# Optimization experiments

Measured on AMD Instinct MI355X. Metric: run time of the kernel, lower is better.

Reference implementation:

```python
import jax, jax.numpy as jnp
import numpy as np

N_NODES = 10000
N_EDGES = 80000
N_GRAPHS = 64
H, D = 4, 512          # num_heads, out_feats
EMB = 768
HFEAT = 512
NCLS = 2
SLOPE = 0.2            # DGL GATConv default negative_slope
BN_EPS = 1e-5


def setup_inputs() -> dict:
    key = jax.random.key(0)
    ks = jax.random.split(key, 24)
    f32 = jnp.float32
    rn = lambda k, s, sc=0.02: jax.random.normal(k, s, dtype=f32) * sc
    inp = {
        "node_feat": jax.random.normal(ks[0], (N_NODES, EMB), dtype=f32),
        "func_feat": jax.random.normal(ks[1], (N_NODES, EMB), dtype=f32),
        "W1": rn(ks[2], (EMB, H * D)),
        "al1": rn(ks[3], (H, D), 0.1),
        "ar1": rn(ks[4], (H, D), 0.1),
        "b1": jnp.zeros((H * D,), f32),
        "W2": rn(ks[5], (H * D, H * D)),
        "al2": rn(ks[6], (H, D), 0.1),
        "ar2": rn(ks[7], (H, D), 0.1),
        "b2": jnp.zeros((H * D,), f32),
        "Wfc": rn(ks[8], (H * D, HFEAT)),
        "bfc": jnp.zeros((HFEAT,), f32),
        "Wfco": rn(ks[9], (EMB, HFEAT)),
        "bfco": jnp.zeros((HFEAT,), f32),
        "Wh": rn(ks[10], (8, HFEAT, HFEAT)),
        "bh": jnp.zeros((8, HFEAT), f32),
        "gamma": jnp.ones((HFEAT,), f32),
        "beta": jnp.zeros((HFEAT,), f32),
        "Whfc": rn(ks[11], (HFEAT, HFEAT)),
        "bhfc": jnp.zeros((HFEAT,), f32),
        "Wf": rn(ks[12], (HFEAT, NCLS)),
        "bf": jnp.zeros((NCLS,), f32),
        "src": jax.random.randint(ks[13], (N_EDGES,), 0, N_NODES),
        "dst": jax.random.randint(ks[14], (N_EDGES,), 0, N_NODES),
        "graph_id": jnp.sort(jax.random.randint(ks[15], (N_NODES,), 0, N_GRAPHS)),
    }
    return inp


def gat_conv(h, W, al, ar, b, src, dst):
    """DGL GATConv (eval mode): fc -> per-head attention logits -> edge
    softmax over incoming edges -> scatter-sum -> +bias. Returns (N, H*D)."""
    feat = (h @ W).reshape(-1, H, D)                      # (N,H,D)
    el = jnp.einsum('nhd,hd->nh', feat, al)               # (N,H)
    er = jnp.einsum('nhd,hd->nh', feat, ar)
    e = jax.nn.leaky_relu(el[src] + er[dst], SLOPE)       # (E,H)
    emax = jax.ops.segment_max(e, dst, num_segments=N_NODES)
    ex = jnp.exp(e - emax[dst])
    den = jax.ops.segment_sum(ex, dst, num_segments=N_NODES)
    a = ex / den[dst]                                     # edge softmax (E,H)
    msg = feat[src] * a[:, :, None]                       # (E,H,D) gather+weight
    out = jax.ops.segment_sum(msg, dst, num_segments=N_NODES)
    return (out + b.reshape(1, H, D)).reshape(-1, H * D)


def reference(node_feat, func_feat, W1, al1, ar1, b1, W2, al2, ar2, b2,
              Wfc, bfc, Wfco, bfco, Wh, bh, gamma, beta, Whfc, bhfc,
              Wf, bf, src, dst, graph_id):
    h = gat_conv(node_feat, W1, al1, ar1, b1, src, dst)   # (N, 2048)
    h = gat_conv(h, W2, al2, ar2, b2, src, dst)           # (N, 2048)
    h = jax.nn.elu(h @ Wfc + bfc)                         # (N, 512)
    h_func = jax.nn.elu(func_feat @ Wfco + bfco)          # (N, 512)
    for i in range(8):
        h = jax.nn.elu(h @ Wh[i] + bh[i])
        h_func = jax.nn.elu(h_func @ Wh[i] + bh[i])       # dead for output (as in torch)
    counts = jax.ops.segment_sum(jnp.ones((N_NODES,), h.dtype), graph_id,
                                 num_segments=N_GRAPHS)
    hg = jax.ops.segment_sum(h, graph_id, num_segments=N_GRAPHS)
    hg = hg / jnp.maximum(counts, 1.0)[:, None]           # dgl.mean_nodes (G, 512)
    # BatchNorm1d eval with running_mean=0, running_var=1
    hg = hg / jnp.sqrt(1.0 + BN_EPS) * gamma + beta
    hg = jax.nn.elu(hg @ Whfc + bhfc)
    return hg @ Wf + bf                                   # (G, NCLS)
```

## Files before the change

kernel.cpp:

```cpp
#include <hip/hip_runtime.h>
#include <hip/hip_bf16.h>
#include <math.h>

#define N_NODES 10000
#define N_EDGES 80000
#define N_GRAPHS 64
#define NH 4
#define HD 512
#define HDTOT 2048
#define EMB 768
#define HFEAT 512
#define MAXDEG 512

typedef _Float16 half8 __attribute__((ext_vector_type(8)));
typedef _Float16 half4 __attribute__((ext_vector_type(4)));
typedef float f32x4 __attribute__((ext_vector_type(4)));

__device__ __forceinline__ void gload_lds16(const void* g, void* l) {
  __builtin_amdgcn_global_load_lds(
      (const __attribute__((address_space(1))) unsigned int*)g,
      (__attribute__((address_space(3))) unsigned int*)l, 16, 0, 0);
}

template <int BM>
__global__ __launch_bounds__(256) void gemm_f16_kernel(
    const _Float16* __restrict__ A, const _Float16* __restrict__ BT,
    const float* __restrict__ bias, _Float16* __restrict__ C,
    int M, int N, int K, int act) {
  constexpr int WR = (BM == 128) ? 2 : 1;
  constexpr int WC = 4 / WR;
  constexpr int MI = (BM / WR) / 16;
  constexpr int NI = (128 / WC) / 16;
  constexpr int NW = NI * 16;
  constexpr int CS = NW + 4;
  constexpr int GPR = NW / 8;

  __shared__ _Float16 smem[(BM + 128) * 64];
  _Float16* As = smem;
  _Float16* Bs = smem + BM * 64;

  const int bn = blockIdx.x * 128, bm = blockIdx.y * BM;
  const int t = threadIdx.x;
  const int lane = t & 63, wave = t >> 6;
  const int wr = wave / WC, wc = wave % WC;
  const int m0 = wr * (BM / WR), n0 = wc * NW;
  const int fr = lane & 15, fq = lane >> 4;

  f32x4 acc[MI][NI];
#pragma unroll
  for (int i = 0; i < MI; ++i)
#pragma unroll
    for (int j = 0; j < NI; ++j) acc[i][j] = (f32x4){0.f, 0.f, 0.f, 0.f};

  for (int k0 = 0; k0 < K; k0 += 64) {
    __syncthreads();
#pragma unroll
    for (int it = 0; it < BM / 32; ++it) {
      int gid = it * 256 + t;
      int r = gid >> 3;
      int q = (gid & 7) ^ (r & 7);
      int grow = bm + r;
      if (grow >= M) grow = M - 1;
      gload_lds16(A + (size_t)grow * K + k0 + q * 8,
                  &As[(it * 256 + wave * 64) * 8]);
    }
#pragma unroll
    for (int it = 0; it < 4; ++it) {
      int gid = it * 256 + t;
      int r = gid >> 3;
      int q = (gid & 7) ^ (r & 7);
      gload_lds16(BT + (size_t)(bn + r) * K + k0 + q * 8,
                  &Bs[(it * 256 + wave * 64) * 8]);
    }
    __syncthreads();

#pragma unroll
    for (int kk = 0; kk < 2; ++kk) {
      half8 af[MI], bf[NI];
#pragma unroll
      for (int mi = 0; mi < MI; ++mi) {
        int m = m0 + mi * 16 + fr;
        af[mi] = *(const half8*)&As[m * 64 + (((kk * 4 + fq) ^ (m & 7))) * 8];
      }
#pragma unroll
      for (int ni = 0; ni < NI; ++ni) {
        int n = n0 + ni * 16 + fr;
        bf[ni] = *(const half8*)&Bs[n * 64 + (((kk * 4 + fq) ^ (n & 7))) * 8];
      }
#pragma unroll
      for (int mi = 0; mi < MI; ++mi)
#pragma unroll
        for (int ni = 0; ni < NI; ++ni)
          acc[mi][ni] = __builtin_amdgcn_mfma_f32_16x16x32_f16(
              af[mi], bf[ni], acc[mi][ni], 0, 0, 0);
    }
  }
  __syncthreads();
  _Float16* cs = smem + wave * 16 * CS;
#pragma unroll
  for (int mi = 0; mi < MI; ++mi) {
#pragma unroll
    for (int ni = 0; ni < NI; ++ni) {
      float bb = bias ? bias[bn + n0 + ni * 16 + fr] : 0.f;
#pragma unroll
      for (int j = 0; j < 4; ++j) {
        float v = acc[mi][ni][j] + bb;
        if (act == 1) v = v > 0.f ? v : expm1f(v);
        cs[(fq * 4 + j) * CS + ni * 16 + fr] = (_Float16)v;
      }
    }
#pragma unroll
    for (int i = 0; i < NW / 32; ++i) {
      int piece = i * 64 + lane;
      int r = piece / GPR, g = piece % GPR;
      int grow = bm + m0 + mi * 16 + r;
      if (grow < M) {
        half8 v = *(const half8*)&cs[r * CS + g * 8];
        *(half8*)&C[(size_t)grow * N + bn + n0 + g * 8] = v;
      }
    }
  }
}

__global__ __launch_bounds__(256) void convert_wt_kernel(
    const float* __restrict__ W, _Float16* __restrict__ WT, int K, int N) {
  __shared__ float tile[32][33];
  W += (size_t)blockIdx.z * K * N;
  WT += (size_t)blockIdx.z * K * N;
  int k0 = blockIdx.x * 32, n0 = blockIdx.y * 32;
  int t = threadIdx.x;
  int r = t >> 3, c4 = (t & 7) * 4;
  float4 v = *(const float4*)(W + (size_t)(k0 + r) * N + n0 + c4);
  tile[r][c4 + 0] = v.x;
  tile[r][c4 + 1] = v.y;
  tile[r][c4 + 2] = v.z;
  tile[r][c4 + 3] = v.w;
  __syncthreads();
  float x0 = tile[c4 + 0][r], x1 = tile[c4 + 1][r];
  float x2 = tile[c4 + 2][r], x3 = tile[c4 + 3][r];
  size_t o = (size_t)(n0 + r) * K + k0 + c4;
  *(half4*)&WT[o] = (half4){(_Float16)x0, (_Float16)x1, (_Float16)x2, (_Float16)x3};
}

__global__ void convert_f32_f16_kernel(const float* __restrict__ x,
                                       _Float16* __restrict__ y, int n4) {
  int gid = blockIdx.x * blockDim.x + threadIdx.x;
  if (gid >= n4) return;
  float4 v = *(const float4*)(x + gid * 4);
  *(half4*)(y + gid * 4) =
      (half4){(_Float16)v.x, (_Float16)v.y, (_Float16)v.z, (_Float16)v.w};
}

__global__ void hist_kernel(const int* __restrict__ dst, int* __restrict__ cnt, int E) {
  int gid = blockIdx.x * blockDim.x + threadIdx.x;
  if (gid < E) atomicAdd(&cnt[dst[gid]], 1);
}

__global__ void scan_kernel(const int* __restrict__ cnt, int* __restrict__ row_ptr,
                            int* __restrict__ cursor, int n) {
  __shared__ int part[256];
  int t = threadIdx.x;
  int chunk = (n + 255) / 256;
  int s0 = t * chunk;
  int s1 = min(s0 + chunk, n);
  int sum = 0;
  for (int i = s0; i < s1; ++i) sum += cnt[i];
  part[t] = sum;
  __syncthreads();
  if (t == 0) {
    int acc = 0;
    for (int i = 0; i < 256; ++i) { int v = part[i]; part[i] = acc; acc += v; }
    row_ptr[n] = acc;
  }
  __syncthreads();
  int run = part[t];
  for (int i = s0; i < s1; ++i) {
    row_ptr[i] = run;
    cursor[i] = run;
    run += cnt[i];
  }
}

__global__ void scatter_kernel(const int* __restrict__ src, const int* __restrict__ dst,
                               int* __restrict__ cursor, int* __restrict__ csr_src,
                               int E) {
  int gid = blockIdx.x * blockDim.x + threadIdx.x;
  if (gid < E) {
    int d = dst[gid];
    int pos = atomicAdd(&cursor[d], 1);
    csr_src[pos] = src[gid];
  }
}

__global__ __launch_bounds__(256) void el_er_kernel(
    const _Float16* __restrict__ feat, const float* __restrict__ al,
    const float* __restrict__ ar, float* __restrict__ el, float* __restrict__ er) {
  int n = blockIdx.x;
  int t = threadIdx.x;
  int h = t >> 6, lane = t & 63;
  half8 f = *(const half8*)(feat + (size_t)n * HDTOT + h * HD + lane * 8);
  const float* ap = al + h * HD + lane * 8;
  const float* rp = ar + h * HD + lane * 8;
  float4 a0 = *(const float4*)ap, a1 = *(const float4*)(ap + 4);
  float4 r0 = *(const float4*)rp, r1 = *(const float4*)(rp + 4);
  float f0 = (float)f[0], f1 = (float)f[1], f2 = (float)f[2], f3 = (float)f[3];
  float f4 = (float)f[4], f5 = (float)f[5], f6 = (float)f[6], f7 = (float)f[7];
  float sl = f0 * a0.x + f1 * a0.y + f2 * a0.z + f3 * a0.w +
             f4 * a1.x + f5 * a1.y + f6 * a1.z + f7 * a1.w;
  float sr = f0 * r0.x + f1 * r0.y + f2 * r0.z + f3 * r0.w +
             f4 * r1.x + f5 * r1.y + f6 * r1.z + f7 * r1.w;
  for (int off = 32; off; off >>= 1) {
    sl += __shfl_down(sl, off);
    sr += __shfl_down(sr, off);
  }
  if (lane == 0) {
    el[n * NH + h] = sl;
    er[n * NH + h] = sr;
  }
}

__global__ __launch_bounds__(256) void softmax_aggregate_kernel(
    const _Float16* __restrict__ feat, const float* __restrict__ el,
    const float* __restrict__ er, const int* __restrict__ row_ptr,
    const int* __restrict__ csr_src, float* __restrict__ e_buf,
    const float* __restrict__ bias, _Float16* __restrict__ out) {
  __shared__ float wl[NH][MAXDEG];
  int n = blockIdx.x;
  int t = threadIdx.x;
  int h = t >> 6, lane = t & 63;
  int s = row_ptr[n], epos = row_ptr[n + 1];
  int deg = epos - s;
  bool lds_w = (deg <= MAXDEG);

  if (deg > 0) {
    float ern = er[n * NH + h];
    if (deg <= 64) {
      int p = s + lane;
      bool on = lane < deg;
      float logit = 0.f;
      float m = -INFINITY;
      if (on) {
        float v = el[csr_src[p] * NH + h] + ern;
        logit = v >= 0.f ? v : 0.2f * v;
        m = logit;
      }
#pragma unroll
      for (int off = 32; off; off >>= 1) m = fmaxf(m, __shfl_xor(m, off));
      float ex = on ? expf(logit - m) : 0.f;
      float sum = ex;
#pragma unroll
      for (int off = 32; off; off >>= 1) sum += __shfl_xor(sum, off);
      float inv = 1.f / sum;
      if (on) wl[h][lane] = ex * inv;
    } else if (lds_w) {
      float m = -INFINITY;
      for (int p = s + lane; p < epos; p += 64) {
        float v = el[csr_src[p] * NH + h] + ern;
        v = v >= 0.f ? v : 0.2f * v;
        wl[h][p - s] = v;
        m = fmaxf(m, v);
      }
      for (int off = 32; off; off >>= 1) m = fmaxf(m, __shfl_xor(m, off));
      float sum = 0.f;
      for (int p = s + lane; p < epos; p += 64) {
        float ex = expf(wl[h][p - s] - m);
        wl[h][p - s] = ex;
        sum += ex;
      }
      for (int off = 32; off; off >>= 1) sum += __shfl_xor(sum, off);
      float inv = 1.f / sum;
      for (int p = s + lane; p < epos; p += 64) wl[h][p - s] *= inv;
    } else {
      float m = -INFINITY;
      for (int p = s + lane; p < epos; p += 64) {
        float v = el[csr_src[p] * NH + h] + ern;
        v = v >= 0.f ? v : 0.2f * v;
        e_buf[p * NH + h] = v;
        m = fmaxf(m, v);
      }
      for (int off = 32; off; off >>= 1) m = fmaxf(m, __shfl_xor(m, off));
      float sum = 0.f;
      for (int p = s + lane; p < epos; p += 64) {
        float ex = expf(e_buf[p * NH + h] - m);
        e_buf[p * NH + h] = ex;
        sum += ex;
      }
      for (int off = 32; off; off >>= 1) sum += __shfl_xor(sum, off);
      float inv = 1.f / sum;
      for (int p = s + lane; p < epos; p += 64) e_buf[p * NH + h] *= inv;
    }
  }
  __syncthreads();

  int base = t * 8;
  float acc[8] = {0.f, 0.f, 0.f, 0.f, 0.f, 0.f, 0.f, 0.f};
  int p = s;
  for (; p + 4 <= epos; p += 4) {
    int q = p - s;
    int sn0 = csr_src[p + 0], sn1 = csr_src[p + 1];
    int sn2 = csr_src[p + 2], sn3 = csr_src[p + 3];
    float a0 = lds_w ? wl[h][q + 0] : e_buf[(p + 0) * NH + h];
    float a1 = lds_w ? wl[h][q + 1] : e_buf[(p + 1) * NH + h];
    float a2 = lds_w ? wl[h][q + 2] : e_buf[(p + 2) * NH + h];
    float a3 = lds_w ? wl[h][q + 3] : e_buf[(p + 3) * NH + h];
    half8 f0 = *(const half8*)(feat + (size_t)sn0 * HDTOT + base);
    half8 f1 = *(const half8*)(feat + (size_t)sn1 * HDTOT + base);
    half8 f2 = *(const half8*)(feat + (size_t)sn2 * HDTOT + base);
    half8 f3 = *(const half8*)(feat + (size_t)sn3 * HDTOT + base);
#pragma unroll
    for (int i = 0; i < 8; ++i)
      acc[i] += a0 * (float)f0[i] + a1 * (float)f1[i] +
                a2 * (float)f2[i] + a3 * (float)f3[i];
  }
  for (; p < epos; ++p) {
    int sn = csr_src[p];
    float a = lds_w ? wl[h][p - s] : e_buf[p * NH + h];
    half8 f = *(const half8*)(feat + (size_t)sn * HDTOT + base);
#pragma unroll
    for (int i = 0; i < 8; ++i) acc[i] += a * (float)f[i];
  }
  float4 b0 = *(const float4*)(bias + base);
  float4 b1 = *(const float4*)(bias + base + 4);
  half8 o;
  o[0] = (_Float16)(acc[0] + b0.x); o[1] = (_Float16)(acc[1] + b0.y);
  o[2] = (_Float16)(acc[2] + b0.z); o[3] = (_Float16)(acc[3] + b0.w);
  o[4] = (_Float16)(acc[4] + b1.x); o[5] = (_Float16)(acc[5] + b1.y);
  o[6] = (_Float16)(acc[6] + b1.z); o[7] = (_Float16)(acc[7] + b1.w);
  *(half8*)(out + (size_t)n * HDTOT + base) = o;
}

__global__ __launch_bounds__(512) void pool_final_kernel(
    const _Float16* __restrict__ hfeat, const int* __restrict__ graph_id,
    const float* __restrict__ gamma, const float* __restrict__ beta,
    const float* __restrict__ Whfc, const float* __restrict__ bhfc,
    const float* __restrict__ Wf, const float* __restrict__ bf,
    float* __restrict__ out) {
  __shared__ float sh[HFEAT];
  __shared__ float st[HFEAT];
  __shared__ float r0[8], r1[8];
  __shared__ int s_lo, s_hi;
  int g = blockIdx.x, t = threadIdx.x;
  if (t == 0) {
    int lo = 0, hi = N_NODES;
    while (lo < hi) { int m = (lo + hi) >> 1; if (graph_id[m] < g) lo = m + 1; else hi = m; }
    s_lo = lo;
    int lo2 = lo, hi2 = N_NODES;
    while (lo2 < hi2) { int m = (lo2 + hi2) >> 1; if (graph_id[m] < g + 1) lo2 = m + 1; else hi2 = m; }
    s_hi = lo2;
  }
  __syncthreads();
  int lo = s_lo, hi = s_hi;
  int col = t;
  float acc = 0.f;
  for (int n = lo; n < hi; ++n) acc += (float)hfeat[(size_t)n * HFEAT + col];
  float invc = 1.f / fmaxf((float)(hi - lo), 1.f);
  float bnscale = rsqrtf(1.f + 1e-5f);
  sh[col] = acc * invc * bnscale * gamma[col] + beta[col];
  __syncthreads();
  float a2 = bhfc[col];
  for (int k = 0; k < HFEAT; ++k) a2 += sh[k] * Whfc[k * HFEAT + col];
  st[col] = a2 > 0.f ? a2 : expm1f(a2);
  __syncthreads();
  float p0 = st[col] * Wf[col * 2 + 0];
  float p1 = st[col] * Wf[col * 2 + 1];
  for (int off = 32; off; off >>= 1) {
    p0 += __shfl_down(p0, off);
    p1 += __shfl_down(p1, off);
  }
  int w = t >> 6;
  if ((t & 63) == 0) { r0[w] = p0; r1[w] = p1; }
  __syncthreads();
  if (t == 0) {
    float q0 = bf[0], q1 = bf[1];
#pragma unroll
    for (int i = 0; i < 8; ++i) { q0 += r0[i]; q1 += r1[i]; }
    out[g * 2 + 0] = q0;
    out[g * 2 + 1] = q1;
  }
}

static void gemm_raw(const _Float16* A, const _Float16* wt, const float* bias,
                     _Float16* C, int M, int N, int K, int act,
                     bool small_m_tile, hipStream_t stream) {
  if (small_m_tile) {
    dim3 grid(N / 128, (M + 63) / 64);
    hipLaunchKernelGGL(gemm_f16_kernel<64>, grid, dim3(256), 0, stream,
                       A, wt, bias, C, M, N, K, act);
  } else {
    dim3 grid(N / 128, (M + 127) / 128);
    hipLaunchKernelGGL(gemm_f16_kernel<128>, grid, dim3(256), 0, stream,
                       A, wt, bias, C, M, N, K, act);
  }
}

static void gemm(const _Float16* A, const float* W, _Float16* wt,
                 const float* bias, _Float16* C, int M, int N, int K, int act,
                 bool small_m_tile, hipStream_t stream) {
  hipLaunchKernelGGL(convert_wt_kernel, dim3(K / 32, N / 32, 1), dim3(256),
                     0, stream, W, wt, K, N);
  gemm_raw(A, wt, bias, C, M, N, K, act, small_m_tile, stream);
}

static void gat_layer(const _Float16* h_in, int K_in, const float* W, _Float16* wt,
                      const float* al, const float* ar, const float* b,
                      const int* row_ptr, const int* csr_src,
                      _Float16* featbuf, float* el, float* er,
                      float* e_buf, _Float16* out, hipStream_t stream) {
  gemm(h_in, W, wt, nullptr, featbuf, N_NODES, HDTOT, K_in, 0, false, stream);
  hipLaunchKernelGGL(el_er_kernel, dim3(N_NODES), dim3(256), 0, stream, featbuf, al, ar, el, er);
  hipLaunchKernelGGL(softmax_aggregate_kernel, dim3(N_NODES), dim3(256), 0, stream,
                     featbuf, el, er, row_ptr, csr_src, e_buf, b, out);
}

extern "C" void kernel_launch(void* const* d_in, const int* in_sizes, int n_in,
                              void* d_out, int out_size, void* d_ws, size_t ws_size,
                              hipStream_t stream) {
  const float* node_feat = (const float*)d_in[0];
  const float* W1 = (const float*)d_in[2];
  const float* al1 = (const float*)d_in[3];
  const float* ar1 = (const float*)d_in[4];
  const float* b1 = (const float*)d_in[5];
  const float* W2 = (const float*)d_in[6];
  const float* al2 = (const float*)d_in[7];
  const float* ar2 = (const float*)d_in[8];
  const float* b2 = (const float*)d_in[9];
  const float* Wfc = (const float*)d_in[10];
  const float* bfc = (const float*)d_in[11];
  const float* Wh = (const float*)d_in[14];
  const float* bh = (const float*)d_in[15];
  const float* gamma = (const float*)d_in[16];
  const float* beta = (const float*)d_in[17];
  const float* Whfc = (const float*)d_in[18];
  const float* bhfc = (const float*)d_in[19];
  const float* Wf = (const float*)d_in[20];
  const float* bf = (const float*)d_in[21];
  const int* src = (const int*)d_in[22];
  const int* dst = (const int*)d_in[23];
  const int* graph_id = (const int*)d_in[24];
  float* out = (float*)d_out;

  _Float16* P0 = (_Float16*)d_ws;
  _Float16* P1 = P0 + (size_t)N_NODES * HDTOT;
  _Float16* Pin = P1 + (size_t)N_NODES * HDTOT;
  _Float16* wt = Pin + (size_t)N_NODES * EMB;
  _Float16* whh = wt + (size_t)2048 * 2048;
  float* el = (float*)(whh + (size_t)8 * HFEAT * HFEAT);
  float* er = el + N_NODES * NH;
  float* e_buf = er + N_NODES * NH;
  int* cnt = (int*)(e_buf + (size_t)N_EDGES * NH);
  int* row_ptr = cnt + N_NODES;
  int* cursor = row_ptr + N_NODES + 1;
  int* csr_src = cursor + N_NODES;

  hipMemsetAsync(cnt, 0, N_NODES * sizeof(int), stream);
  hipLaunchKernelGGL(hist_kernel, dim3((N_EDGES + 255) / 256), dim3(256), 0, stream,
                     dst, cnt, N_EDGES);
  hipLaunchKernelGGL(scan_kernel, dim3(1), dim3(256), 0, stream, cnt, row_ptr, cursor, N_NODES);
  hipLaunchKernelGGL(scatter_kernel, dim3((N_EDGES + 255) / 256), dim3(256), 0, stream,
                     src, dst, cursor, csr_src, N_EDGES);

  int n4 = N_NODES * EMB / 4;
  hipLaunchKernelGGL(convert_f32_f16_kernel, dim3((n4 + 255) / 256), dim3(256), 0, stream,
                     node_feat, Pin, n4);
  hipLaunchKernelGGL(convert_wt_kernel, dim3(HFEAT / 32, HFEAT / 32, 8),
                     dim3(256), 0, stream, Wh, whh, HFEAT, HFEAT);

  gat_layer(Pin, EMB, W1, wt, al1, ar1, b1, row_ptr, csr_src,
            P0, el, er, e_buf, P1, stream);
  gat_layer(P1, HDTOT, W2, wt, al2, ar2, b2, row_ptr, csr_src,
            P0, el, er, e_buf, P1, stream);

  gemm(P1, Wfc, wt, bfc, P0, N_NODES, HFEAT, HDTOT, 1, true, stream);

  _Float16* cur = P0;
  _Float16* nxt = P1;
  for (int i = 0; i < 8; ++i) {
    gemm_raw(cur, whh + (size_t)i * HFEAT * HFEAT, bh + (size_t)i * HFEAT, nxt,
             N_NODES, HFEAT, HFEAT, 1, true, stream);
    _Float16* tmp = cur; cur = nxt; nxt = tmp;
  }

  hipLaunchKernelGGL(pool_final_kernel, dim3(N_GRAPHS), dim3(512), 0, stream,
                     cur, graph_id, gamma, beta, Whfc, bhfc, Wf, bf, out);
}
```

Before: 704.8 us.

## Add 256x256-tile four-stage pipelined GEMM for GAT projection layers

After: 729.4 us. 1.03x slower.

```diff
diff --git a/kernel.cpp b/kernel.cpp
--- a/kernel.cpp
+++ b/kernel.cpp
@@ -20,6 +20,17 @@
   __builtin_amdgcn_global_load_lds(
       (const __attribute__((address_space(1))) unsigned int*)g,
       (__attribute__((address_space(3))) unsigned int*)l, 16, 0, 0);
+}
+
+__device__ __forceinline__ void wgbar() {
+  asm volatile("" ::: "memory");
+  __builtin_amdgcn_s_barrier();
+  asm volatile("" ::: "memory");
+}
+
+template <int N>
+__device__ __forceinline__ void vmwait() {
+  asm volatile("s_waitcnt vmcnt(%0)" ::"n"(N) : "memory");
 }
 
 template <int BM>
@@ -113,6 +124,133 @@
     for (int i = 0; i < NW / 32; ++i) {
       int piece = i * 64 + lane;
       int r = piece / GPR, g = piece % GPR;
+      int grow = bm + m0 + mi * 16 + r;
+      if (grow < M) {
+        half8 v = *(const half8*)&cs[r * CS + g * 8];
+        *(half8*)&C[(size_t)grow * N + bn + n0 + g * 8] = v;
+      }
+    }
+  }
+}
+
+#define G256_SLOT 16384
+
+__global__ __launch_bounds__(512, 2) void gemm256_f16_kernel(
+    const _Float16* __restrict__ A, const _Float16* __restrict__ BT,
+    const float* __restrict__ bias, _Float16* __restrict__ C,
+    int M, int N, int K, int act, int nbx) {
+  __shared__ _Float16 smem[4 * G256_SLOT];
+
+  int flat = blockIdx.x;
+  int nwg = gridDim.x;
+  if ((nwg & 7) == 0) flat = (flat & 7) * (nwg >> 3) + (flat >> 3);
+  const int bn = (flat % nbx) * 256;
+  const int bm = (flat / nbx) * 256;
+
+  const int t = threadIdx.x;
+  const int lane = t & 63, wave = t >> 6;
+  const int wr = wave >> 2, wc = wave & 3;
+  const int m0 = wr * 128, n0 = wc * 64;
+  const int fr = lane & 15, fq = lane >> 4;
+
+  const _Float16* srcA[2];
+  const _Float16* srcB[2];
+#pragma unroll
+  for (int it = 0; it < 2; ++it) {
+    int gi = it * 512 + t;
+    int r = gi >> 2;
+    int g = (gi & 3) ^ ((r >> 1) & 3);
+    int ra = bm + r;
+    if (ra >= M) ra = M - 1;
+    srcA[it] = A + (size_t)ra * K + g * 8;
+    srcB[it] = BT + (size_t)(bn + r) * K + g * 8;
+  }
+
+  int offA[8], offB[4];
+#pragma unroll
+  for (int mi = 0; mi < 8; ++mi) {
+    int m = m0 + mi * 16 + fr;
+    offA[mi] = m * 32 + ((fq ^ ((m >> 1) & 3)) << 3);
+  }
+#pragma unroll
+  for (int ni = 0; ni < 4; ++ni) {
+    int n = n0 + ni * 16 + fr;
+    offB[ni] = 8192 + n * 32 + ((fq ^ ((n >> 1) & 3)) << 3);
+  }
+
+  f32x4 acc[8][4];
+#pragma unroll
+  for (int i = 0; i < 8; ++i)
+#pragma unroll
+    for (int j = 0; j < 4; ++j) acc[i][j] = (f32x4){0.f, 0.f, 0.f, 0.f};
+
+  const int ldsbase = (wave * 64) * 8;
+
+#define G256_STAGE(kt, slot)                                               \
+  do {                                                                     \
+    _Float16* sA_ = smem + (slot)*G256_SLOT;                               \
+    _Float16* sB_ = sA_ + 8192;                                            \
+    gload_lds16(srcA[0] + (size_t)(kt)*32, &sA_[ldsbase]);                 \
+    gload_lds16(srcA[1] + (size_t)(kt)*32, &sA_[4096 + ldsbase]);          \
+    gload_lds16(srcB[0] + (size_t)(kt)*32, &sB_[ldsbase]);                 \
+    gload_lds16(srcB[1] + (size_t)(kt)*32, &sB_[4096 + ldsbase]);          \
+  } while (0)
+
+  const int NT = K >> 5;
+
+  G256_STAGE(0, 0);
+  G256_STAGE(1, 1);
+  G256_STAGE(2, 2);
+  vmwait<8>();
+  wgbar();
+
+  for (int tt = 0; tt < NT; ++tt) {
+    if (tt + 3 < NT) G256_STAGE(tt + 3, (tt + 3) & 3);
+
+    const _Float16* sl = smem + (tt & 3) * G256_SLOT;
+    half8 af[8], bf[4];
+#pragma unroll
+    for (int mi = 0; mi < 8; ++mi) af[mi] = *(const half8*)&sl[offA[mi]];
+#pragma unroll
+    for (int ni = 0; ni < 4; ++ni) bf[ni] = *(const half8*)&sl[offB[ni]];
+
+    __builtin_amdgcn_s_setprio(1);
+#pragma unroll
+    for (int mi = 0; mi < 8; ++mi)
+#pragma unroll
+      for (int ni = 0; ni < 4; ++ni)
+        acc[mi][ni] = __builtin_amdgcn_mfma_f32_16x16x32_f16(
+            af[mi], bf[ni], acc[mi][ni], 0, 0, 0);
+    __builtin_amdgcn_s_setprio(0);
+
+    if (tt + 3 < NT)
+      vmwait<8>();
+    else if (tt + 2 < NT)
+      vmwait<4>();
+    else if (tt + 1 < NT)
+      vmwait<0>();
+    wgbar();
+  }
+#undef G256_STAGE
+
+  constexpr int CS = 68;
+  _Float16* cs = smem + wave * 16 * CS;
+#pragma unroll
+  for (int mi = 0; mi < 8; ++mi) {
+#pragma unroll
+    for (int ni = 0; ni < 4; ++ni) {
+      float bb = bias ? bias[bn + n0 + ni * 16 + fr] : 0.f;
+#pragma unroll
+      for (int j = 0; j < 4; ++j) {
+        float v = acc[mi][ni][j] + bb;
+        if (act == 1) v = v > 0.f ? v : expm1f(v);
+        cs[(fq * 4 + j) * CS + ni * 16 + fr] = (_Float16)v;
+      }
+    }
+#pragma unroll
+    for (int i = 0; i < 2; ++i) {
+      int piece = i * 64 + lane;
+      int r = piece >> 3, g = piece & 7;
       int grow = bm + m0 + mi * 16 + r;
       if (grow < M) {
         half8 v = *(const half8*)&cs[r * CS + g * 8];
@@ -401,12 +539,22 @@
   gemm_raw(A, wt, bias, C, M, N, K, act, small_m_tile, stream);
 }
 
+static void gemm_big(const _Float16* A, const float* W, _Float16* wt,
+                     const float* bias, _Float16* C, int M, int N, int K,
+                     int act, hipStream_t stream) {
+  hipLaunchKernelGGL(convert_wt_kernel, dim3(K / 32, N / 32, 1), dim3(256),
+                     0, stream, W, wt, K, N);
+  int nbx = N / 256, nby = (M + 255) / 256;
+  hipLaunchKernelGGL(gemm256_f16_kernel, dim3(nbx * nby), dim3(512), 0, stream,
+                     A, wt, bias, C, M, N, K, act, nbx);
+}
+
 static void gat_layer(const _Float16* h_in, int K_in, const float* W, _Float16* wt,
                       const float* al, const float* ar, const float* b,
                       const int* row_ptr, const int* csr_src,
                       _Float16* featbuf, float* el, float* er,
                       float* e_buf, _Float16* out, hipStream_t stream) {
-  gemm(h_in, W, wt, nullptr, featbuf, N_NODES, HDTOT, K_in, 0, false, stream);
+  gemm_big(h_in, W, wt, nullptr, featbuf, N_NODES, HDTOT, K_in, 0, stream);
   hipLaunchKernelGGL(el_er_kernel, dim3(N_NODES), dim3(256), 0, stream, featbuf, al, ar, el, er);
   hipLaunchKernelGGL(softmax_aggregate_kernel, dim3(N_NODES), dim3(256), 0, stream,
                      featbuf, el, er, row_ptr, csr_src, e_buf, b, out);
```

## Fuse eight hidden-layer GEMMs into one kernel keeping row tile in LDS

Applied to the files above, without the earlier changes.

After: 854.9 us. +21.3%, slower.

```diff
diff --git a/kernel.cpp b/kernel.cpp
--- a/kernel.cpp
+++ b/kernel.cpp
@@ -120,6 +120,106 @@
       }
     }
   }
+}
+
+#define HB 32
+
+__global__ __launch_bounds__(256) void hidden8_kernel(
+    const _Float16* __restrict__ in,
+    const _Float16* __restrict__ FB,
+    const float* __restrict__ bh,
+    _Float16* __restrict__ outp) {
+  __shared__ _Float16 IT[HB * 512];
+  const int bm = blockIdx.x * HB;
+  const int t = threadIdx.x;
+  const int lane = t & 63, wc = t >> 6;
+  const int fr = lane & 15, fq = lane >> 4;
+
+#pragma unroll
+  for (int k = 0; k < 8; ++k) {
+    int gi = k * 256 + t;
+    int r = gi >> 6, g = gi & 63;
+    int grow = bm + r;
+    if (grow >= N_NODES) grow = N_NODES - 1;
+    half8 v = *(const half8*)&in[(size_t)grow * HFEAT + g * 8];
+    *(half8*)&IT[r * HFEAT + ((g ^ (r & 7)) << 3)] = v;
+  }
+  __syncthreads();
+
+#pragma unroll 1
+  for (int l = 0; l < 8; ++l) {
+    f32x4 acc[2][8];
+#pragma unroll
+    for (int mi = 0; mi < 2; ++mi)
+#pragma unroll
+      for (int ni = 0; ni < 8; ++ni) acc[mi][ni] = (f32x4){0.f, 0.f, 0.f, 0.f};
+
+    const _Float16* fb = FB + (size_t)l * (16 * 32 * 512);
+#pragma unroll 2
+    for (int ks = 0; ks < 16; ++ks) {
+      half8 af[2];
+#pragma unroll
+      for (int mi = 0; mi < 2; ++mi) {
+        int m = mi * 16 + fr;
+        af[mi] = *(const half8*)&IT[m * HFEAT + (((ks * 4 + fq) ^ (m & 7)) << 3)];
+      }
+      half8 bf[8];
+#pragma unroll
+      for (int ni = 0; ni < 8; ++ni)
+        bf[ni] = *(const half8*)&fb[((size_t)ks * 32 + wc * 8 + ni) * 512 + lane * 8];
+#pragma unroll
+      for (int mi = 0; mi < 2; ++mi)
+#pragma unroll
+        for (int ni = 0; ni < 8; ++ni)
+          acc[mi][ni] = __builtin_amdgcn_mfma_f32_16x16x32_f16(
+              af[mi], bf[ni], acc[mi][ni], 0, 0, 0);
+    }
+    __syncthreads();
+#pragma unroll
+    for (int mi = 0; mi < 2; ++mi)
+#pragma unroll
+      for (int ni = 0; ni < 8; ++ni) {
+        int c = wc * 128 + ni * 16 + fr;
+        float bb = bh[l * 512 + c];
+#pragma unroll
+        for (int j = 0; j < 4; ++j) {
+          float v = acc[mi][ni][j] + bb;
+          v = v > 0.f ? v : expm1f(v);
+          int r = mi * 16 + fq * 4 + j;
+          IT[r * HFEAT + ((((c >> 3) ^ (r & 7)) << 3) | (c & 7))] = (_Float16)v;
+        }
+      }
+    __syncthreads();
+  }
+
+#pragma unroll
+  for (int k = 0; k < 8; ++k) {
+    int gi = k * 256 + t;
+    int r = gi >> 6, g = gi & 63;
+    int grow = bm + r;
+    if (grow < N_NODES) {
+      half8 v = *(const half8*)&IT[r * HFEAT + ((g ^ (r & 7)) << 3)];
+      *(half8*)&outp[(size_t)grow * HFEAT + g * 8] = v;
+    }
+  }
+}
+
+__global__ __launch_bounds__(256) void convert_fb_kernel(
+    const float* __restrict__ Wh, _Float16* __restrict__ FB) {
+  int gid = blockIdx.x * 256 + threadIdx.x;
+  int l = gid >> 15;
+  int rem = gid & 32767;
+  int ks = rem >> 11;
+  int rem2 = rem & 2047;
+  int nf = rem2 >> 6;
+  int lane = rem2 & 63;
+  int fr = lane & 15, fq = lane >> 4;
+  const float* w = Wh + (size_t)l * 512 * 512;
+  half8 v;
+#pragma unroll
+  for (int j = 0; j < 8; ++j)
+    v[j] = (_Float16)w[(size_t)(ks * 32 + fq * 8 + j) * 512 + nf * 16 + fr];
+  *(half8*)&FB[(size_t)gid * 8] = v;
 }
 
 __global__ __launch_bounds__(256) void convert_wt_kernel(
@@ -443,8 +543,8 @@
   _Float16* P1 = P0 + (size_t)N_NODES * HDTOT;
   _Float16* Pin = P1 + (size_t)N_NODES * HDTOT;
   _Float16* wt = Pin + (size_t)N_NODES * EMB;
-  _Float16* whh = wt + (size_t)2048 * 2048;
-  float* el = (float*)(whh + (size_t)8 * HFEAT * HFEAT);
+  _Float16* FB = wt + (size_t)2048 * 2048;
+  float* el = (float*)(FB + (size_t)8 * HFEAT * HFEAT);
   float* er = el + N_NODES * NH;
   float* e_buf = er + N_NODES * NH;
   int* cnt = (int*)(e_buf + (size_t)N_EDGES * NH);
@@ -462,8 +562,7 @@
   int n4 = N_NODES * EMB / 4;
   hipLaunchKernelGGL(convert_f32_f16_kernel, dim3((n4 + 255) / 256), dim3(256), 0, stream,
                      node_feat, Pin, n4);
-  hipLaunchKernelGGL(convert_wt_kernel, dim3(HFEAT / 32, HFEAT / 32, 8),
-                     dim3(256), 0, stream, Wh, whh, HFEAT, HFEAT);
+  hipLaunchKernelGGL(convert_fb_kernel, dim3(1024), dim3(256), 0, stream, Wh, FB);
 
   gat_layer(Pin, EMB, W1, wt, al1, ar1, b1, row_ptr, csr_src,
             P0, el, er, e_buf, P1, stream);
@@ -472,14 +571,9 @@
 
   gemm(P1, Wfc, wt, bfc, P0, N_NODES, HFEAT, HDTOT, 1, true, stream);
 
-  _Float16* cur = P0;
-  _Float16* nxt = P1;
-  for (int i = 0; i < 8; ++i) {
-    gemm_raw(cur, whh + (size_t)i * HFEAT * HFEAT, bh + (size_t)i * HFEAT, nxt,
-             N_NODES, HFEAT, HFEAT, 1, true, stream);
-    _Float16* tmp = cur; cur = nxt; nxt = tmp;
-  }
+  hipLaunchKernelGGL(hidden8_kernel, dim3((N_NODES + HB - 1) / HB), dim3(256),
+                     0, stream, P0, FB, bh, P1);
 
   hipLaunchKernelGGL(pool_final_kernel, dim3(N_GRAPHS), dim3(512), 0, stream,
-                     cur, graph_id, gamma, beta, Whfc, bhfc, Wf, bf, out);
-}
+                     P1, graph_id, gamma, beta, Whfc, bhfc, Wf, bf, out);
+}
```

## Fuse eight hidden-layer GEMMs into one cooperative persistent kernel with grid sync

Applied to the files above, without the earlier changes.

Result: no change. 716.8 us (+1.7%).

```diff
diff --git a/kernel.cpp b/kernel.cpp
--- a/kernel.cpp
+++ b/kernel.cpp
@@ -1,6 +1,9 @@
 #include <hip/hip_runtime.h>
+#include <hip/hip_cooperative_groups.h>
 #include <hip/hip_bf16.h>
 #include <math.h>
+
+namespace cg = cooperative_groups;
 
 #define N_NODES 10000
 #define N_EDGES 80000
@@ -118,6 +121,109 @@
         half8 v = *(const half8*)&cs[r * CS + g * 8];
         *(half8*)&C[(size_t)grow * N + bn + n0 + g * 8] = v;
       }
+    }
+  }
+}
+
+__global__ __launch_bounds__(256) void hidden_chain_coop(
+    _Float16* __restrict__ b0, _Float16* __restrict__ b1,
+    const _Float16* __restrict__ whh, const float* __restrict__ bh) {
+  constexpr int MI = 4, NI = 2, NW = 32, CS = 36;
+  __shared__ _Float16 smem[(64 + 128) * 64];
+  _Float16* As = smem;
+  _Float16* Bs = smem + 64 * 64;
+
+  const int tile = blockIdx.x;
+  const int bn = (tile & 3) * 128;
+  const int bm = (tile >> 2) * 64;
+  const int t = threadIdx.x;
+  const int lane = t & 63, wave = t >> 6;
+  const int n0 = wave * NW;
+  const int fr = lane & 15, fq = lane >> 4;
+
+  for (int l = 0; l < 8; ++l) {
+    const _Float16* A = (l & 1) ? b1 : b0;
+    _Float16* C = (l & 1) ? b0 : b1;
+    const _Float16* BT = whh + (size_t)l * (HFEAT * HFEAT);
+    const float* bias = bh + l * HFEAT;
+
+    f32x4 acc[MI][NI];
+#pragma unroll
+    for (int i = 0; i < MI; ++i)
+#pragma unroll
+      for (int j = 0; j < NI; ++j) acc[i][j] = (f32x4){0.f, 0.f, 0.f, 0.f};
+
+    for (int k0 = 0; k0 < HFEAT; k0 += 64) {
+      __syncthreads();
+#pragma unroll
+      for (int it = 0; it < 2; ++it) {
+        int gid = it * 256 + t;
+        int r = gid >> 3;
+        int q = (gid & 7) ^ (r & 7);
+        int grow = bm + r;
+        if (grow >= N_NODES) grow = N_NODES - 1;
+        gload_lds16(A + (size_t)grow * HFEAT + k0 + q * 8,
+                    &As[(it * 256 + wave * 64) * 8]);
+      }
+#pragma unroll
+      for (int it = 0; it < 4; ++it) {
+        int gid = it * 256 + t;
+        int r = gid >> 3;
+        int q = (gid & 7) ^ (r & 7);
+        gload_lds16(BT + (size_t)(bn + r) * HFEAT + k0 + q * 8,
+                    &Bs[(it * 256 + wave * 64) * 8]);
+      }
+      __syncthreads();
+
+#pragma unroll
+      for (int kk = 0; kk < 2; ++kk) {
+        half8 af[MI], bf[NI];
+#pragma unroll
+        for (int mi = 0; mi < MI; ++mi) {
+          int m = mi * 16 + fr;
+          af[mi] = *(const half8*)&As[m * 64 + (((kk * 4 + fq) ^ (m & 7))) * 8];
+        }
+#pragma unroll
+        for (int ni = 0; ni < NI; ++ni) {
+          int n = n0 + ni * 16 + fr;
+          bf[ni] = *(const half8*)&Bs[n * 64 + (((kk * 4 + fq) ^ (n & 7))) * 8];
+        }
+#pragma unroll
+        for (int mi = 0; mi < MI; ++mi)
+#pragma unroll
+          for (int ni = 0; ni < NI; ++ni)
+            acc[mi][ni] = __builtin_amdgcn_mfma_f32_16x16x32_f16(
+                af[mi], bf[ni], acc[mi][ni], 0, 0, 0);
+      }
+    }
+    __syncthreads();
+
+    _Float16* cs = smem + wave * 16 * CS;
+#pragma unroll
+    for (int mi = 0; mi < MI; ++mi) {
+#pragma unroll
+      for (int ni = 0; ni < NI; ++ni) {
+        float bb = bias[bn + n0 + ni * 16 + fr];
+#pragma unroll
+        for (int j = 0; j < 4; ++j) {
+          float v = acc[mi][ni][j] + bb;
+          v = v > 0.f ? v : expm1f(v);
+          cs[(fq * 4 + j) * CS + ni * 16 + fr] = (_Float16)v;
+        }
+      }
+      {
+        int r = lane >> 2, g = lane & 3;
+        int grow = bm + mi * 16 + r;
+        if (grow < N_NODES) {
+          half8 v = *(const half8*)&cs[r * CS + g * 8];
+          *(half8*)&C[(size_t)grow * HFEAT + bn + n0 + g * 8] = v;
+        }
+      }
+    }
+
+    if (l < 7) {
+      __threadfence();
+      cg::this_grid().sync();
     }
   }
 }
@@ -410,6 +516,17 @@
   hipLaunchKernelGGL(el_er_kernel, dim3(N_NODES), dim3(256), 0, stream, featbuf, al, ar, el, er);
   hipLaunchKernelGGL(softmax_aggregate_kernel, dim3(N_NODES), dim3(256), 0, stream,
                      featbuf, el, er, row_ptr, csr_src, e_buf, b, out);
+}
+
+static bool hidden_coop_ok() {
+  static int cached = -1;
+  if (cached < 0) {
+    int maxb = 0;
+    hipError_t e = hipOccupancyMaxActiveBlocksPerMultiprocessor(
+        &maxb, hidden_chain_coop, 256, 0);
+    cached = (e == hipSuccess && maxb >= 3) ? 1 : 0;
+  }
+  return cached == 1;
 }
 
 extern "C" void kernel_launch(void* const* d_in, const int* in_sizes, int n_in,
@@ -472,14 +589,24 @@
 
   gemm(P1, Wfc, wt, bfc, P0, N_NODES, HFEAT, HDTOT, 1, true, stream);
 
-  _Float16* cur = P0;
-  _Float16* nxt = P1;
-  for (int i = 0; i < 8; ++i) {
-    gemm_raw(cur, whh + (size_t)i * HFEAT * HFEAT, bh + (size_t)i * HFEAT, nxt,
-             N_NODES, HFEAT, HFEAT, 1, true, stream);
-    _Float16* tmp = cur; cur = nxt; nxt = tmp;
+  if (hidden_coop_ok()) {
+    _Float16* a0 = P0;
+    _Float16* a1 = P1;
+    const _Float16* wp = whh;
+    const float* bp = bh;
+    void* args[] = {&a0, &a1, &wp, &bp};
+    hipLaunchCooperativeKernel((const void*)hidden_chain_coop, dim3(628),
+                               dim3(256), args, 0, stream);
+  } else {
+    _Float16* cur = P0;
+    _Float16* nxt = P1;
+    for (int i = 0; i < 8; ++i) {
+      gemm_raw(cur, whh + (size_t)i * HFEAT * HFEAT, bh + (size_t)i * HFEAT,
+               nxt, N_NODES, HFEAT, HFEAT, 1, true, stream);
+      _Float16* tmp = cur; cur = nxt; nxt = tmp;
+    }
   }
 
   hipLaunchKernelGGL(pool_final_kernel, dim3(N_GRAPHS), dim3(512), 0, stream,
-                     cur, graph_id, gamma, beta, Whfc, bhfc, Wf, bf, out);
-}
+                     P0, graph_id, gamma, beta, Whfc, bhfc, Wf, bf, out);
+}
```
